# Optimization experiments

Hardware: AMD Instinct MI355X
Metric: run time of the kernel (lower is better)

The kernel has to match this reference:

```python
import jax, jax.numpy as jnp
import numpy as np

N = 100000      # nodes
E = 1600000     # edges (avg degree 16)
IN = 128        # in_channels
HID = 32        # hidden_channels per head
HEADS = 4
OUT = 64        # out_channels
NEG_SLOPE = 0.2 # PyG GATConv default leaky_relu slope


def setup_inputs() -> dict:
    key = jax.random.key(0)
    ks = jax.random.split(key, 12)
    def glorot(k, shape):
        fan = shape[0] + shape[-1]
        s = jnp.sqrt(6.0 / fan)
        return jax.random.uniform(k, shape, jnp.float32, -s, s)
    return {
        "x": jax.random.normal(ks[0], (N, IN), jnp.float32),
        "edge_index": jax.random.randint(ks[1], (2, E), 0, N, dtype=jnp.int64),
        # GATConv layer 1: in=IN, out=HID per head, heads=HEADS, concat=True
        "W1": glorot(ks[2], (IN, HEADS * HID)),
        "a_src1": glorot(ks[3], (HEADS, HID)),
        "a_dst1": glorot(ks[4], (HEADS, HID)),
        "b1": jnp.zeros((HEADS * HID,), jnp.float32),
        # GATConv layer 2: in=HEADS*HID, out=OUT, heads=1, concat=False
        "W2": glorot(ks[5], (HEADS * HID, OUT)),
        "a_src2": glorot(ks[6], (1, OUT)),
        "a_dst2": glorot(ks[7], (1, OUT)),
        "b2": jnp.zeros((OUT,), jnp.float32),
    }


def _gat_layer(x, src, dst, W, a_src, a_dst, bias, num_nodes, concat):
    """PyG-style GATConv (add_self_loops already applied to src/dst).
    x: [N, F_in]; src/dst: [E']; W: [F_in, H*C]; a_*: [H, C]."""
    H, C = a_src.shape
    h = (x @ W).reshape(-1, H, C)                       # [N, H, C]
    # per-node attention scores (avoid gathering full features for logits)
    e_src = (h * a_src[None]).sum(-1)                   # [N, H]
    e_dst = (h * a_dst[None]).sum(-1)                   # [N, H]
    logits = jax.nn.leaky_relu(e_src[src] + e_dst[dst], NEG_SLOPE)  # [E', H]
    # segment softmax over incoming edges of each destination node
    mx = jax.ops.segment_max(logits, dst, num_segments=num_nodes)   # [N, H]
    ex = jnp.exp(logits - mx[dst])                      # [E', H]
    den = jax.ops.segment_sum(ex, dst, num_segments=num_nodes)      # [N, H]
    alpha = ex / (den[dst] + 1e-16)                     # [E', H]
    # weighted message aggregation
    msg = h[src] * alpha[..., None]                     # [E', H, C]
    out = jax.ops.segment_sum(msg, dst, num_segments=num_nodes)     # [N, H, C]
    if concat:
        out = out.reshape(num_nodes, H * C)
    else:
        out = out.mean(axis=1)
    return out + bias


def reference(x, edge_index, W1, a_src1, a_dst1, b1, W2, a_src2, a_dst2, b2):
    n = x.shape[0]
    loops = jnp.arange(n, dtype=edge_index.dtype)
    src = jnp.concatenate([edge_index[0], loops])       # add self-loops (PyG default)
    dst = jnp.concatenate([edge_index[1], loops])
    # dropout layers are identity in eval mode
    h = _gat_layer(x, src, dst, W1, a_src1, a_dst1, b1, n, concat=True)
    h = jax.nn.elu(h)
    out = _gat_layer(h, src, dst, W2, a_src2, a_dst2, b2, n, concat=False)
    return out
```

## Files before the change

### kernel.cpp

```cpp
#include <hip/hip_runtime.h>
#include <cmath>

#define IN_F 128
#define HID 32
#define HEADS 4
#define OUT_F 64
#define NEG_SLOPE 0.2f
#define MAXSEG 128
#define BSHIFT 7
#define NBMAX 1024
#define CHUNK 8192
#define LDSTRIDE 136

typedef short bfrag8 __attribute__((ext_vector_type(8)));
typedef float facc4 __attribute__((ext_vector_type(4)));

__device__ __forceinline__ int ldidx(const int* ei, int pos, int is64) {
  return is64 ? ei[2 * pos] : ei[pos];
}
__device__ __forceinline__ unsigned short f2b(float f) {
  unsigned u = __float_as_uint(f);
  u += 0x7fffu + ((u >> 16) & 1u);
  return (unsigned short)(u >> 16);
}
__device__ __forceinline__ float b2f_lo(unsigned u) { return __uint_as_float(u << 16); }
__device__ __forceinline__ float b2f_hi(unsigned u) { return __uint_as_float(u & 0xffff0000u); }
__device__ __forceinline__ void wave_lds_fence() {
  asm volatile("s_waitcnt lgkmcnt(0)" ::: "memory");
}

__global__ __launch_bounds__(256) void detect_kernel(const int* __restrict__ ei, int E, int* __restrict__ flag) {
  __shared__ int red[256];
  int acc = 0;
  int limit = E < 4096 ? E : 4096;
  for (int j = threadIdx.x; j < limit; j += 256) acc |= ei[2 * j + 1];
  red[threadIdx.x] = acc;
  __syncthreads();
  for (int s = 128; s > 0; s >>= 1) {
    if ((int)threadIdx.x < s) red[threadIdx.x] |= red[threadIdx.x + s];
    __syncthreads();
  }
  if (threadIdx.x == 0) *flag = (red[0] == 0) ? 1 : 0;
}

__global__ __launch_bounds__(256) void bcount_kernel(const int* __restrict__ ei, int E, int Etot,
                                                     const int* __restrict__ flag, int NB,
                                                     int* __restrict__ bcnt) {
  __shared__ int hcnt[NBMAX];
  int tid = threadIdx.x;
  int base = blockIdx.x * CHUNK;
  int cnt = Etot - base; if (cnt > CHUNK) cnt = CHUNK;
  int is64 = *flag;
  for (int i = tid; i < NB; i += 256) hcnt[i] = 0;
  __syncthreads();
  for (int i = tid; i < cnt; i += 256) {
    int e = base + i;
    int d = (e < E) ? ldidx(ei, E + e, is64) : (e - E);
    atomicAdd(&hcnt[d >> BSHIFT], 1);
  }
  __syncthreads();
  for (int i = tid; i < NB; i += 256) {
    int c = hcnt[i];
    if (c) atomicAdd(&bcnt[i], c);
  }
}

__global__ __launch_bounds__(1024) void bscan_kernel(const int* __restrict__ bcnt,
                                                     int* __restrict__ bptr, int* __restrict__ bcur, int NB) {
  __shared__ int wsum[16];
  int tid = threadIdx.x, lane = tid & 63, w = tid >> 6;
  int v = (tid < NB) ? bcnt[tid] : 0;
  int incl = v;
  #pragma unroll
  for (int off = 1; off < 64; off <<= 1) { int t = __shfl_up(incl, off); if (lane >= off) incl += t; }
  if (lane == 63) wsum[w] = incl;
  __syncthreads();
  if (w == 0) {
    int s = (lane < 16) ? wsum[lane] : 0;
    #pragma unroll
    for (int off = 1; off < 16; off <<= 1) { int t = __shfl_up(s, off); if (lane >= off) s += t; }
    if (lane < 16) wsum[lane] = s;
  }
  __syncthreads();
  if (w > 0) incl += wsum[w - 1];
  int excl = incl - v;
  if (tid < NB) { bptr[tid] = excl; bcur[tid] = excl; }
  if (tid == 1023) bptr[NB] = incl;
}

__global__ __launch_bounds__(256) void bscatter_kernel(const int* __restrict__ ei, int E, int Etot,
                                                       const int* __restrict__ flag, int NB,
                                                       int* __restrict__ bcur, uint2* __restrict__ ebuf) {
  __shared__ int hcnt[NBMAX];
  __shared__ int hcur[NBMAX];
  int tid = threadIdx.x;
  int base = blockIdx.x * CHUNK;
  int cnt = Etot - base; if (cnt > CHUNK) cnt = CHUNK;
  int is64 = *flag;
  for (int i = tid; i < NB; i += 256) hcnt[i] = 0;
  __syncthreads();
  for (int i = tid; i < cnt; i += 256) {
    int e = base + i;
    int d = (e < E) ? ldidx(ei, E + e, is64) : (e - E);
    atomicAdd(&hcnt[d >> BSHIFT], 1);
  }
  __syncthreads();
  for (int i = tid; i < NB; i += 256) {
    int c = hcnt[i];
    hcur[i] = c ? atomicAdd(&bcur[i], c) : 0;
  }
  __syncthreads();
  for (int i = tid; i < cnt; i += 256) {
    int e = base + i;
    int s, d;
    if (e < E) { s = ldidx(ei, e, is64); d = ldidx(ei, E + e, is64); }
    else       { s = e - E; d = s; }
    int pos = atomicAdd(&hcur[d >> BSHIFT], 1);
    ebuf[pos] = make_uint2((unsigned)s, (unsigned)d);
  }
}

__global__ __launch_bounds__(256) void bcsr_kernel(const int* __restrict__ bptr, const uint2* __restrict__ ebuf,
                                                   int* __restrict__ rowptr, int* __restrict__ csr,
                                                   int N, int NB) {
  __shared__ int cnt[128];
  __shared__ int cur[128];
  __shared__ int w0sum;
  int tid = threadIdx.x;
  int b = blockIdx.x;
  int lo = bptr[b], hi = bptr[b + 1];
  int node0 = b << BSHIFT;
  int nn = N - node0; if (nn > 128) nn = 128;
  if (tid < 128) cnt[tid] = 0;
  __syncthreads();
  for (int i = lo + tid; i < hi; i += 256) {
    atomicAdd(&cnt[ebuf[i].y & 127], 1);
  }
  __syncthreads();
  int v = 0, incl = 0;
  if (tid < 128) {
    v = cnt[tid];
    incl = v;
    int lane = tid & 63;
    #pragma unroll
    for (int off = 1; off < 64; off <<= 1) { int t = __shfl_up(incl, off); if (lane >= off) incl += t; }
    if (tid == 63) w0sum = incl;
  }
  __syncthreads();
  if (tid < 128) {
    if (tid >= 64) incl += w0sum;
    int excl = incl - v;
    cur[tid] = excl;
    if (tid < nn) rowptr[node0 + tid] = lo + excl;
  }
  if (b == NB - 1 && tid == 0) rowptr[N] = hi;
  __syncthreads();
  for (int i = lo + tid; i < hi; i += 256) {
    uint2 pr = ebuf[i];
    int p = atomicAdd(&cur[pr.y & 127], 1);
    csr[lo + p] = (int)pr.x;
  }
}

__global__ __launch_bounds__(256) void gemm1_kernel(
    const float* __restrict__ x, const float* __restrict__ W,
    const float* __restrict__ asr, const float* __restrict__ ads,
    unsigned short* __restrict__ h1b, float* __restrict__ es, float* __restrict__ ed,
    int N) {
  __shared__ short Wt[128 * LDSTRIDE];
  __shared__ short As[64 * LDSTRIDE];
  int tid = threadIdx.x;
  int row0 = blockIdx.x * 64;
  int lane = tid & 63, wv = tid >> 6;
  int m2 = lane & 15, quad = lane >> 4;

  for (int i = tid; i < 128 * 128; i += 256) {
    int k = i >> 7, c = i & 127;
    Wt[c * LDSTRIDE + k] = (short)f2b(W[i]);
  }
  for (int idx = tid; idx < 64 * 16; idx += 256) {
    int r = idx >> 4, ch = idx & 15;
    int n = row0 + r;
    bfrag8 sv;
    if (n < N) {
      float4 v0 = *(const float4*)&x[(size_t)n * 128 + ch * 8];
      float4 v1 = *(const float4*)&x[(size_t)n * 128 + ch * 8 + 4];
      sv[0] = (short)f2b(v0.x); sv[1] = (short)f2b(v0.y);
      sv[2] = (short)f2b(v0.z); sv[3] = (short)f2b(v0.w);
      sv[4] = (short)f2b(v1.x); sv[5] = (short)f2b(v1.y);
      sv[6] = (short)f2b(v1.z); sv[7] = (short)f2b(v1.w);
    } else {
      sv = (bfrag8)0;
    }
    *(bfrag8*)&As[r * LDSTRIDE + ch * 8] = sv;
  }
  __syncthreads();

  facc4 acc[8] = {};
  const short* Abase = &As[(wv * 16 + m2) * LDSTRIDE];
  #pragma unroll
  for (int ks = 0; ks < 4; ++ks) {
    int k = ks * 32 + quad * 8;
    bfrag8 af = *(const bfrag8*)&Abase[k];
    #pragma unroll
    for (int t = 0; t < 8; ++t) {
      bfrag8 bf = *(const bfrag8*)&Wt[(t * 16 + m2) * LDSTRIDE + k];
      acc[t] = __builtin_amdgcn_mfma_f32_16x16x32_bf16(af, bf, acc[t], 0, 0, 0);
    }
  }

  float av[8], bv[8];
  #pragma unroll
  for (int t = 0; t < 8; ++t) {
    int ai = (t >> 1) * 32 + (t & 1) * 16 + m2;
    av[t] = asr[ai]; bv[t] = ads[ai];
  }
  #pragma unroll
  for (int r = 0; r < 4; ++r) {
    int n = row0 + wv * 16 + quad * 4 + r;
    bool valid = (n < N);
    if (valid) {
      #pragma unroll
      for (int t = 0; t < 8; ++t)
        h1b[(size_t)n * 128 + t * 16 + m2] = f2b(acc[t][r]);
    }
    #pragma unroll
    for (int h = 0; h < 4; ++h) {
      float ps = acc[2 * h][r] * av[2 * h] + acc[2 * h + 1][r] * av[2 * h + 1];
      float pd = acc[2 * h][r] * bv[2 * h] + acc[2 * h + 1][r] * bv[2 * h + 1];
      ps += __shfl_xor(ps, 1); ps += __shfl_xor(ps, 2); ps += __shfl_xor(ps, 4); ps += __shfl_xor(ps, 8);
      pd += __shfl_xor(pd, 1); pd += __shfl_xor(pd, 2); pd += __shfl_xor(pd, 4); pd += __shfl_xor(pd, 8);
      if (valid && m2 == 0) {
        es[(size_t)n * 4 + h] = ps;
        ed[(size_t)n * 4 + h] = pd;
      }
    }
  }
}

__global__ __launch_bounds__(256) void gemm2_kernel(
    const unsigned short* __restrict__ xb, const float* __restrict__ W,
    const float* __restrict__ asr, const float* __restrict__ ads,
    unsigned short* __restrict__ h2b, float* __restrict__ es, float* __restrict__ ed,
    int N) {
  __shared__ short Wt[64 * LDSTRIDE];
  __shared__ short As[64 * LDSTRIDE];
  int tid = threadIdx.x;
  int row0 = blockIdx.x * 64;
  int lane = tid & 63, wv = tid >> 6;
  int m2 = lane & 15, quad = lane >> 4;

  for (int i = tid; i < 128 * 64; i += 256) {
    int k = i >> 6, c = i & 63;
    Wt[c * LDSTRIDE + k] = (short)f2b(W[i]);
  }
  for (int idx = tid; idx < 64 * 16; idx += 256) {
    int r = idx >> 4, ch = idx & 15;
    int n = row0 + r;
    uint4 u = (n < N) ? *(const uint4*)&xb[(size_t)n * 128 + ch * 8]
                      : make_uint4(0, 0, 0, 0);
    *(uint4*)&As[r * LDSTRIDE + ch * 8] = u;
  }
  __syncthreads();

  facc4 acc[4] = {};
  const short* Abase = &As[(wv * 16 + m2) * LDSTRIDE];
  #pragma unroll
  for (int ks = 0; ks < 4; ++ks) {
    int k = ks * 32 + quad * 8;
    bfrag8 af = *(const bfrag8*)&Abase[k];
    #pragma unroll
    for (int t = 0; t < 4; ++t) {
      bfrag8 bf = *(const bfrag8*)&Wt[(t * 16 + m2) * LDSTRIDE + k];
      acc[t] = __builtin_amdgcn_mfma_f32_16x16x32_bf16(af, bf, acc[t], 0, 0, 0);
    }
  }

  float av[4], bv[4];
  #pragma unroll
  for (int t = 0; t < 4; ++t) {
    av[t] = asr[t * 16 + m2]; bv[t] = ads[t * 16 + m2];
  }
  #pragma unroll
  for (int r = 0; r < 4; ++r) {
    int n = row0 + wv * 16 + quad * 4 + r;
    bool valid = (n < N);
    if (valid) {
      #pragma unroll
      for (int t = 0; t < 4; ++t)
        h2b[(size_t)n * 64 + t * 16 + m2] = f2b(acc[t][r]);
    }
    float ps = acc[0][r] * av[0] + acc[1][r] * av[1] + acc[2][r] * av[2] + acc[3][r] * av[3];
    float pd = acc[0][r] * bv[0] + acc[1][r] * bv[1] + acc[2][r] * bv[2] + acc[3][r] * bv[3];
    ps += __shfl_xor(ps, 1); ps += __shfl_xor(ps, 2); ps += __shfl_xor(ps, 4); ps += __shfl_xor(ps, 8);
    pd += __shfl_xor(pd, 1); pd += __shfl_xor(pd, 2); pd += __shfl_xor(pd, 4); pd += __shfl_xor(pd, 8);
    if (valid && m2 == 0) { es[n] = ps; ed[n] = pd; }
  }
}

__global__ __launch_bounds__(256) void agg1_kernel(
    const int* __restrict__ rowptr, const int* __restrict__ csr,
    const float* __restrict__ es, const float* __restrict__ ed,
    const unsigned short* __restrict__ h1b, const float* __restrict__ b1,
    unsigned short* __restrict__ hmidb, int N) {
  __shared__ float lds_p[4][MAXSEG][4];
  __shared__ int   lds_s[4][MAXSEG];
  int wv = threadIdx.x >> 6, lane = threadIdx.x & 63;
  int n = blockIdx.x * 4 + wv;
  if (n >= N) return;
  int start = rowptr[n], end = rowptr[n + 1];
  int len = end - start;
  float4 edv = ((const float4*)ed)[n];
  int f = lane * 2;
  int hh = lane >> 4;
  float ax = 0.f, ay = 0.f;
  const unsigned* h32 = (const unsigned*)h1b;

  if (len <= MAXSEG) {
    float m0 = -1e30f, m1 = -1e30f, m2 = -1e30f, m3 = -1e30f;
    for (int j = lane; j < len; j += 64) {
      int s = csr[start + j];
      lds_s[wv][j] = s;
      float4 ev = ((const float4*)es)[s];
      float l0 = ev.x + edv.x; l0 = l0 > 0.f ? l0 : NEG_SLOPE * l0;
      float l1 = ev.y + edv.y; l1 = l1 > 0.f ? l1 : NEG_SLOPE * l1;
      float l2 = ev.z + edv.z; l2 = l2 > 0.f ? l2 : NEG_SLOPE * l2;
      float l3 = ev.w + edv.w; l3 = l3 > 0.f ? l3 : NEG_SLOPE * l3;
      *(float4*)&lds_p[wv][j][0] = make_float4(l0, l1, l2, l3);
      m0 = fmaxf(m0, l0); m1 = fmaxf(m1, l1); m2 = fmaxf(m2, l2); m3 = fmaxf(m3, l3);
    }
    #pragma unroll
    for (int off = 32; off; off >>= 1) {
      m0 = fmaxf(m0, __shfl_xor(m0, off)); m1 = fmaxf(m1, __shfl_xor(m1, off));
      m2 = fmaxf(m2, __shfl_xor(m2, off)); m3 = fmaxf(m3, __shfl_xor(m3, off));
    }
    float s0 = 0.f, s1 = 0.f, s2 = 0.f, s3 = 0.f;
    for (int j = lane; j < len; j += 64) {
      float4 l = *(float4*)&lds_p[wv][j][0];
      float p0 = __expf(l.x - m0), p1 = __expf(l.y - m1);
      float p2 = __expf(l.z - m2), p3 = __expf(l.w - m3);
      *(float4*)&lds_p[wv][j][0] = make_float4(p0, p1, p2, p3);
      s0 += p0; s1 += p1; s2 += p2; s3 += p3;
    }
    #pragma unroll
    for (int off = 32; off; off >>= 1) {
      s0 += __shfl_xor(s0, off); s1 += __shfl_xor(s1, off);
      s2 += __shfl_xor(s2, off); s3 += __shfl_xor(s3, off);
    }
    float i0 = 1.f / (s0 + 1e-16f), i1 = 1.f / (s1 + 1e-16f);
    float i2 = 1.f / (s2 + 1e-16f), i3 = 1.f / (s3 + 1e-16f);
    float ih = (hh & 2) ? ((hh & 1) ? i3 : i2) : ((hh & 1) ? i1 : i0);
    wave_lds_fence();
    float ax1 = 0.f, ay1 = 0.f;
    int j = 0;
    for (; j + 4 <= len; j += 4) {
      int sA = lds_s[wv][j],     sB = lds_s[wv][j + 1];
      int sC = lds_s[wv][j + 2], sD = lds_s[wv][j + 3];
      float aA = lds_p[wv][j][hh] * ih,     aB = lds_p[wv][j + 1][hh] * ih;
      float aC = lds_p[wv][j + 2][hh] * ih, aD = lds_p[wv][j + 3][hh] * ih;
      unsigned uA = h32[(size_t)sA * 64 + lane];
      unsigned uB = h32[(size_t)sB * 64 + lane];
      unsigned uC = h32[(size_t)sC * 64 + lane];
      unsigned uD = h32[(size_t)sD * 64 + lane];
      ax  = fmaf(b2f_lo(uA), aA, ax);  ay  = fmaf(b2f_hi(uA), aA, ay);
      ax1 = fmaf(b2f_lo(uB), aB, ax1); ay1 = fmaf(b2f_hi(uB), aB, ay1);
      ax  = fmaf(b2f_lo(uC), aC, ax);  ay  = fmaf(b2f_hi(uC), aC, ay);
      ax1 = fmaf(b2f_lo(uD), aD, ax1); ay1 = fmaf(b2f_hi(uD), aD, ay1);
    }
    for (; j < len; ++j) {
      int sA = lds_s[wv][j];
      float aA = lds_p[wv][j][hh] * ih;
      unsigned uA = h32[(size_t)sA * 64 + lane];
      ax = fmaf(b2f_lo(uA), aA, ax);
      ay = fmaf(b2f_hi(uA), aA, ay);
    }
    ax += ax1; ay += ay1;
  } else {
    float m0 = -1e30f, m1 = -1e30f, m2 = -1e30f, m3 = -1e30f;
    for (int j = start + lane; j < end; j += 64) {
      int s = csr[j];
      float4 ev = ((const float4*)es)[s];
      float l0 = ev.x + edv.x; l0 = l0 > 0.f ? l0 : NEG_SLOPE * l0;
      float l1 = ev.y + edv.y; l1 = l1 > 0.f ? l1 : NEG_SLOPE * l1;
      float l2 = ev.z + edv.z; l2 = l2 > 0.f ? l2 : NEG_SLOPE * l2;
      float l3 = ev.w + edv.w; l3 = l3 > 0.f ? l3 : NEG_SLOPE * l3;
      m0 = fmaxf(m0, l0); m1 = fmaxf(m1, l1); m2 = fmaxf(m2, l2); m3 = fmaxf(m3, l3);
    }
    #pragma unroll
    for (int off = 32; off; off >>= 1) {
      m0 = fmaxf(m0, __shfl_xor(m0, off)); m1 = fmaxf(m1, __shfl_xor(m1, off));
      m2 = fmaxf(m2, __shfl_xor(m2, off)); m3 = fmaxf(m3, __shfl_xor(m3, off));
    }
    float s0 = 0.f, s1 = 0.f, s2 = 0.f, s3 = 0.f;
    for (int j = start + lane; j < end; j += 64) {
      int s = csr[j];
      float4 ev = ((const float4*)es)[s];
      float l0 = ev.x + edv.x; l0 = l0 > 0.f ? l0 : NEG_SLOPE * l0;
      float l1 = ev.y + edv.y; l1 = l1 > 0.f ? l1 : NEG_SLOPE * l1;
      float l2 = ev.z + edv.z; l2 = l2 > 0.f ? l2 : NEG_SLOPE * l2;
      float l3 = ev.w + edv.w; l3 = l3 > 0.f ? l3 : NEG_SLOPE * l3;
      s0 += __expf(l0 - m0); s1 += __expf(l1 - m1); s2 += __expf(l2 - m2); s3 += __expf(l3 - m3);
    }
    #pragma unroll
    for (int off = 32; off; off >>= 1) {
      s0 += __shfl_xor(s0, off); s1 += __shfl_xor(s1, off);
      s2 += __shfl_xor(s2, off); s3 += __shfl_xor(s3, off);
    }
    float i0 = 1.f / (s0 + 1e-16f), i1 = 1.f / (s1 + 1e-16f);
    float i2 = 1.f / (s2 + 1e-16f), i3 = 1.f / (s3 + 1e-16f);
    float edh = (hh & 2) ? ((hh & 1) ? edv.w : edv.z) : ((hh & 1) ? edv.y : edv.x);
    float mh = (hh & 2) ? ((hh & 1) ? m3 : m2) : ((hh & 1) ? m1 : m0);
    float ih = (hh & 2) ? ((hh & 1) ? i3 : i2) : ((hh & 1) ? i1 : i0);
    for (int j = start; j < end; ++j) {
      int s = csr[j];
      float l = es[(size_t)s * 4 + hh] + edh; l = l > 0.f ? l : NEG_SLOPE * l;
      float a = __expf(l - mh) * ih;
      unsigned u = h32[(size_t)s * 64 + lane];
      ax = fmaf(b2f_lo(u), a, ax);
      ay = fmaf(b2f_hi(u), a, ay);
    }
  }
  float o0 = ax + b1[f], o1 = ay + b1[f + 1];
  o0 = o0 > 0.f ? o0 : expm1f(o0);
  o1 = o1 > 0.f ? o1 : expm1f(o1);
  unsigned packed = (unsigned)f2b(o0) | ((unsigned)f2b(o1) << 16);
  ((unsigned*)hmidb)[(size_t)n * 64 + lane] = packed;
}

__global__ __launch_bounds__(256) void agg2_kernel(
    const int* __restrict__ rowptr, const int* __restrict__ csr,
    const float* __restrict__ es, const float* __restrict__ ed,
    const unsigned short* __restrict__ h2b, const float* __restrict__ b2,
    float* __restrict__ out, int N) {
  __shared__ float lds_p[4][MAXSEG];
  __shared__ int   lds_s[4][MAXSEG];
  int wv = threadIdx.x >> 6, lane = threadIdx.x & 63;
  int n = blockIdx.x * 4 + wv;
  if (n >= N) return;
  int start = rowptr[n], end = rowptr[n + 1];
  int len = end - start;
  float edv = ed[n];
  float acc = 0.f;

  if (len <= MAXSEG) {
    float m = -1e30f;
    for (int j = lane; j < len; j += 64) {
      int s = csr[start + j];
      lds_s[wv][j] = s;
      float l = es[s] + edv; l = l > 0.f ? l : NEG_SLOPE * l;
      lds_p[wv][j] = l;
      m = fmaxf(m, l);
    }
    #pragma unroll
    for (int off = 32; off; off >>= 1) m = fmaxf(m, __shfl_xor(m, off));
    float sm = 0.f;
    for (int j = lane; j < len; j += 64) {
      float p = __expf(lds_p[wv][j] - m);
      lds_p[wv][j] = p;
      sm += p;
    }
    #pragma unroll
    for (int off = 32; off; off >>= 1) sm += __shfl_xor(sm, off);
    float inv = 1.f / (sm + 1e-16f);
    wave_lds_fence();
    float acc1 = 0.f;
    int j = 0;
    for (; j + 4 <= len; j += 4) {
      int sA = lds_s[wv][j],     sB = lds_s[wv][j + 1];
      int sC = lds_s[wv][j + 2], sD = lds_s[wv][j + 3];
      float aA = lds_p[wv][j] * inv,     aB = lds_p[wv][j + 1] * inv;
      float aC = lds_p[wv][j + 2] * inv, aD = lds_p[wv][j + 3] * inv;
      float vA = __uint_as_float(((unsigned)h2b[(size_t)sA * 64 + lane]) << 16);
      float vB = __uint_as_float(((unsigned)h2b[(size_t)sB * 64 + lane]) << 16);
      float vC = __uint_as_float(((unsigned)h2b[(size_t)sC * 64 + lane]) << 16);
      float vD = __uint_as_float(((unsigned)h2b[(size_t)sD * 64 + lane]) << 16);
      acc  = fmaf(vA, aA, acc);  acc1 = fmaf(vB, aB, acc1);
      acc  = fmaf(vC, aC, acc);  acc1 = fmaf(vD, aD, acc1);
    }
    for (; j < len; ++j) {
      int sA = lds_s[wv][j];
      float aA = lds_p[wv][j] * inv;
      float vA = __uint_as_float(((unsigned)h2b[(size_t)sA * 64 + lane]) << 16);
      acc = fmaf(vA, aA, acc);
    }
    acc += acc1;
  } else {
    float m = -1e30f;
    for (int j = start + lane; j < end; j += 64) {
      float l = es[csr[j]] + edv; l = l > 0.f ? l : NEG_SLOPE * l;
      m = fmaxf(m, l);
    }
    #pragma unroll
    for (int off = 32; off; off >>= 1) m = fmaxf(m, __shfl_xor(m, off));
    float sm = 0.f;
    for (int j = start + lane; j < end; j += 64) {
      float l = es[csr[j]] + edv; l = l > 0.f ? l : NEG_SLOPE * l;
      sm += __expf(l - m);
    }
    #pragma unroll
    for (int off = 32; off; off >>= 1) sm += __shfl_xor(sm, off);
    float inv = 1.f / (sm + 1e-16f);
    for (int j = start; j < end; ++j) {
      int s = csr[j];
      float l = es[s] + edv; l = l > 0.f ? l : NEG_SLOPE * l;
      float a = __expf(l - m) * inv;
      float v = __uint_as_float(((unsigned)h2b[(size_t)s * 64 + lane]) << 16);
      acc = fmaf(v, a, acc);
    }
  }
  out[(size_t)n * 64 + lane] = acc + b2[lane];
}

extern "C" void kernel_launch(void* const* d_in, const int* in_sizes, int n_in,
                              void* d_out, int out_size, void* d_ws, size_t ws_size,
                              hipStream_t stream) {
  const float* x   = (const float*)d_in[0];
  const int*   ei  = (const int*)d_in[1];
  const float* W1  = (const float*)d_in[2];
  const float* as1 = (const float*)d_in[3];
  const float* ad1 = (const float*)d_in[4];
  const float* b1  = (const float*)d_in[5];
  const float* W2  = (const float*)d_in[6];
  const float* as2 = (const float*)d_in[7];
  const float* ad2 = (const float*)d_in[8];
  const float* b2  = (const float*)d_in[9];
  float* out = (float*)d_out;

  int N = in_sizes[0] / IN_F;
  int E = in_sizes[1] / 2;
  int Etot = E + N;
  int NB = (N + 127) >> BSHIFT;

  char* p = (char*)d_ws;
  auto carve = [&](size_t bytes) -> char* {
    char* r = p;
    p += (bytes + 255) & ~(size_t)255;
    return r;
  };
  int* flag     = (int*)carve(4);
  int* bcnt     = (int*)carve((size_t)NBMAX * 4);
  int* bptr     = (int*)carve((size_t)(NBMAX + 1) * 4);
  int* bcur     = (int*)carve((size_t)NBMAX * 4);
  uint2* ebuf   = (uint2*)carve((size_t)Etot * 8);
  int* rowptr   = (int*)carve((size_t)(N + 1) * 4);
  int* csr      = (int*)carve((size_t)Etot * 4);
  float* es1    = (float*)carve((size_t)N * 4 * 4);
  float* ed1    = (float*)carve((size_t)N * 4 * 4);
  float* es2    = (float*)carve((size_t)N * 4);
  float* ed2    = (float*)carve((size_t)N * 4);
  unsigned short* h1b   = (unsigned short*)carve((size_t)N * 128 * 2);
  unsigned short* hmidb = (unsigned short*)carve((size_t)N * 128 * 2);
  unsigned short* h2b   = (unsigned short*)carve((size_t)N * 64 * 2);

  int nchunk = (Etot + CHUNK - 1) / CHUNK;
  hipMemsetAsync(bcnt, 0, (size_t)NB * 4, stream);
  detect_kernel<<<1, 256, 0, stream>>>(ei, E, flag);
  bcount_kernel<<<nchunk, 256, 0, stream>>>(ei, E, Etot, flag, NB, bcnt);
  bscan_kernel<<<1, 1024, 0, stream>>>(bcnt, bptr, bcur, NB);
  bscatter_kernel<<<nchunk, 256, 0, stream>>>(ei, E, Etot, flag, NB, bcur, ebuf);
  bcsr_kernel<<<NB, 256, 0, stream>>>(bptr, ebuf, rowptr, csr, N, NB);
  gemm1_kernel<<<(N + 63) / 64, 256, 0, stream>>>(x, W1, as1, ad1, h1b, es1, ed1, N);
  agg1_kernel<<<(N + 3) / 4, 256, 0, stream>>>(rowptr, csr, es1, ed1, h1b, b1, hmidb, N);
  gemm2_kernel<<<(N + 63) / 64, 256, 0, stream>>>(hmidb, W2, as2, ad2, h2b, es2, ed2, N);
  agg2_kernel<<<(N + 3) / 4, 256, 0, stream>>>(rowptr, csr, es2, ed2, h2b, b2, out, N);
}
```

Measured before the change: 354.9 us.

## Process four nodes per wave in aggregation kernels and pack edge buffer

Both aggregation kernels now give each wave four destination nodes. The softmax runs per 16-lane group, and the gather loop handles two edges at once, with each half-wave reading a wider slice of a feature row. Before, one node per wave wasted most lanes, since the average degree is about 17. The bucket-scatter buffer also packs source and local destination into a single 32-bit word, which halves that traffic. In exchange the code is more complex, and nodes with degree above 64 fall back to a slow serial path that runs after the fast loop.

```diff
diff --git a/kernel.cpp b/kernel.cpp
--- a/kernel.cpp
+++ b/kernel.cpp
@@ -2,11 +2,8 @@
 #include <cmath>
 
 #define IN_F 128
-#define HID 32
-#define HEADS 4
-#define OUT_F 64
 #define NEG_SLOPE 0.2f
-#define MAXSEG 128
+#define SEG 64
 #define BSHIFT 7
 #define NBMAX 1024
 #define CHUNK 8192
@@ -28,6 +25,7 @@
 __device__ __forceinline__ void wave_lds_fence() {
   asm volatile("s_waitcnt lgkmcnt(0)" ::: "memory");
 }
+__device__ __forceinline__ float leaky(float l) { return fmaxf(l, NEG_SLOPE * l); }
 
 __global__ __launch_bounds__(256) void detect_kernel(const int* __restrict__ ei, int E, int* __restrict__ flag) {
   __shared__ int red[256];
@@ -90,7 +88,7 @@
 
 __global__ __launch_bounds__(256) void bscatter_kernel(const int* __restrict__ ei, int E, int Etot,
                                                        const int* __restrict__ flag, int NB,
-                                                       int* __restrict__ bcur, uint2* __restrict__ ebuf) {
+                                                       int* __restrict__ bcur, unsigned* __restrict__ ebuf) {
   __shared__ int hcnt[NBMAX];
   __shared__ int hcur[NBMAX];
   int tid = threadIdx.x;
@@ -116,11 +114,11 @@
     if (e < E) { s = ldidx(ei, e, is64); d = ldidx(ei, E + e, is64); }
     else       { s = e - E; d = s; }
     int pos = atomicAdd(&hcur[d >> BSHIFT], 1);
-    ebuf[pos] = make_uint2((unsigned)s, (unsigned)d);
-  }
-}
-
-__global__ __launch_bounds__(256) void bcsr_kernel(const int* __restrict__ bptr, const uint2* __restrict__ ebuf,
+    ebuf[pos] = ((unsigned)s << 7) | ((unsigned)d & 127u);
+  }
+}
+
+__global__ __launch_bounds__(256) void bcsr_kernel(const int* __restrict__ bptr, const unsigned* __restrict__ ebuf,
                                                    int* __restrict__ rowptr, int* __restrict__ csr,
                                                    int N, int NB) {
   __shared__ int cnt[128];
@@ -134,7 +132,7 @@
   if (tid < 128) cnt[tid] = 0;
   __syncthreads();
   for (int i = lo + tid; i < hi; i += 256) {
-    atomicAdd(&cnt[ebuf[i].y & 127], 1);
+    atomicAdd(&cnt[ebuf[i] & 127u], 1);
   }
   __syncthreads();
   int v = 0, incl = 0;
@@ -156,9 +154,9 @@
   if (b == NB - 1 && tid == 0) rowptr[N] = hi;
   __syncthreads();
   for (int i = lo + tid; i < hi; i += 256) {
-    uint2 pr = ebuf[i];
-    int p = atomicAdd(&cur[pr.y & 127], 1);
-    csr[lo + p] = (int)pr.x;
+    unsigned pr = ebuf[i];
+    int p = atomicAdd(&cur[pr & 127u], 1);
+    csr[lo + p] = (int)(pr >> 7);
   }
 }
 
@@ -301,214 +299,300 @@
 __global__ __launch_bounds__(256) void agg1_kernel(
     const int* __restrict__ rowptr, const int* __restrict__ csr,
     const float* __restrict__ es, const float* __restrict__ ed,
-    const unsigned short* __restrict__ h1b, const float* __restrict__ b1,
+    const unsigned short* __restrict__ h1b, const float* __restrict__ bias1,
     unsigned short* __restrict__ hmidb, int N) {
-  __shared__ float lds_p[4][MAXSEG][4];
-  __shared__ int   lds_s[4][MAXSEG];
-  int wv = threadIdx.x >> 6, lane = threadIdx.x & 63;
-  int n = blockIdx.x * 4 + wv;
-  if (n >= N) return;
-  int start = rowptr[n], end = rowptr[n + 1];
-  int len = end - start;
-  float4 edv = ((const float4*)ed)[n];
-  int f = lane * 2;
-  int hh = lane >> 4;
-  float ax = 0.f, ay = 0.f;
-  const unsigned* h32 = (const unsigned*)h1b;
-
-  if (len <= MAXSEG) {
+  __shared__ float lds_a[4][4][4][SEG + 1];
+  __shared__ int   lds_s[4][4][SEG];
+  int tid = threadIdx.x;
+  int wv = tid >> 6, lane = tid & 63;
+  int sub = lane >> 4, sj = lane & 15;
+  int nbase = blockIdx.x * 16 + wv * 4;
+  int n = nbase + sub;
+  bool nvalid = (n < N);
+  int start = 0, len = 0;
+  if (nvalid) { start = rowptr[n]; len = rowptr[n + 1] - start; }
+  int lenc = (len <= SEG) ? len : 0;
+
+  float4 edv = nvalid ? ((const float4*)ed)[n] : make_float4(0.f, 0.f, 0.f, 0.f);
+  float l[4][4];
+  float mx = -1e30f;
+  #pragma unroll
+  for (int it = 0; it < 4; ++it) {
+    int j = sj + it * 16;
+    if (j < lenc) {
+      int s = csr[start + j];
+      lds_s[wv][sub][j] = s;
+      float4 ev = ((const float4*)es)[s];
+      float l0 = leaky(ev.x + edv.x);
+      float l1 = leaky(ev.y + edv.y);
+      float l2 = leaky(ev.z + edv.z);
+      float l3 = leaky(ev.w + edv.w);
+      l[it][0] = l0; l[it][1] = l1; l[it][2] = l2; l[it][3] = l3;
+      mx = fmaxf(mx, fmaxf(fmaxf(l0, l1), fmaxf(l2, l3)));
+    } else {
+      l[it][0] = -1e30f; l[it][1] = -1e30f; l[it][2] = -1e30f; l[it][3] = -1e30f;
+    }
+  }
+  #pragma unroll
+  for (int off = 1; off < 16; off <<= 1) mx = fmaxf(mx, __shfl_xor(mx, off));
+
+  float s0 = 0.f, s1 = 0.f, s2 = 0.f, s3 = 0.f;
+  #pragma unroll
+  for (int it = 0; it < 4; ++it) {
+    float p0 = __expf(l[it][0] - mx);
+    float p1 = __expf(l[it][1] - mx);
+    float p2 = __expf(l[it][2] - mx);
+    float p3 = __expf(l[it][3] - mx);
+    l[it][0] = p0; l[it][1] = p1; l[it][2] = p2; l[it][3] = p3;
+    s0 += p0; s1 += p1; s2 += p2; s3 += p3;
+  }
+  #pragma unroll
+  for (int off = 1; off < 16; off <<= 1) {
+    s0 += __shfl_xor(s0, off); s1 += __shfl_xor(s1, off);
+    s2 += __shfl_xor(s2, off); s3 += __shfl_xor(s3, off);
+  }
+  float i0 = __builtin_amdgcn_rcpf(s0 + 1e-16f);
+  float i1 = __builtin_amdgcn_rcpf(s1 + 1e-16f);
+  float i2 = __builtin_amdgcn_rcpf(s2 + 1e-16f);
+  float i3 = __builtin_amdgcn_rcpf(s3 + 1e-16f);
+  #pragma unroll
+  for (int it = 0; it < 4; ++it) {
+    int j = sj + it * 16;
+    if (j < lenc) {
+      lds_a[wv][sub][0][j] = l[it][0] * i0;
+      lds_a[wv][sub][1][j] = l[it][1] * i1;
+      lds_a[wv][sub][2][j] = l[it][2] * i2;
+      lds_a[wv][sub][3][j] = l[it][3] * i3;
+    }
+  }
+  if (sj == 0 && (lenc & 1)) {
+    lds_s[wv][sub][lenc] = 0;
+    lds_a[wv][sub][0][lenc] = 0.f; lds_a[wv][sub][1][lenc] = 0.f;
+    lds_a[wv][sub][2][lenc] = 0.f; lds_a[wv][sub][3][lenc] = 0.f;
+  }
+  wave_lds_fence();
+
+  int fl = lane & 31, eidx = lane >> 5, hd = fl >> 3;
+  const uint2* hrow = (const uint2*)h1b;
+  #pragma unroll 1
+  for (int i = 0; i < 4; ++i) {
+    int lenC = __shfl(lenc, i << 4);
+    if (lenC == 0) continue;
+    int nI = nbase + i;
+    const float* aP = &lds_a[wv][i][hd][0];
+    const int*   sP = &lds_s[wv][i][0];
+    int lenp = (lenC + 1) & ~1;
+    float c0 = 0.f, c1 = 0.f, c2 = 0.f, c3 = 0.f;
+    float d0 = 0.f, d1 = 0.f, d2 = 0.f, d3 = 0.f;
+    int g = 0;
+    for (; g + 4 <= lenp; g += 4) {
+      int sA = sP[g + eidx],     sB = sP[g + 2 + eidx];
+      float wA = aP[g + eidx],   wB = aP[g + 2 + eidx];
+      uint2 uA = hrow[(size_t)sA * 32 + fl];
+      uint2 uB = hrow[(size_t)sB * 32 + fl];
+      c0 = fmaf(b2f_lo(uA.x), wA, c0); c1 = fmaf(b2f_hi(uA.x), wA, c1);
+      c2 = fmaf(b2f_lo(uA.y), wA, c2); c3 = fmaf(b2f_hi(uA.y), wA, c3);
+      d0 = fmaf(b2f_lo(uB.x), wB, d0); d1 = fmaf(b2f_hi(uB.x), wB, d1);
+      d2 = fmaf(b2f_lo(uB.y), wB, d2); d3 = fmaf(b2f_hi(uB.y), wB, d3);
+    }
+    if (g < lenp) {
+      int sA = sP[g + eidx];
+      float wA = aP[g + eidx];
+      uint2 uA = hrow[(size_t)sA * 32 + fl];
+      c0 = fmaf(b2f_lo(uA.x), wA, c0); c1 = fmaf(b2f_hi(uA.x), wA, c1);
+      c2 = fmaf(b2f_lo(uA.y), wA, c2); c3 = fmaf(b2f_hi(uA.y), wA, c3);
+    }
+    c0 += d0; c1 += d1; c2 += d2; c3 += d3;
+    c0 += __shfl_xor(c0, 32); c1 += __shfl_xor(c1, 32);
+    c2 += __shfl_xor(c2, 32); c3 += __shfl_xor(c3, 32);
+    if (eidx == 0) {
+      float4 bb = *(const float4*)&bias1[fl * 4];
+      float o0 = c0 + bb.x, o1 = c1 + bb.y, o2 = c2 + bb.z, o3 = c3 + bb.w;
+      o0 = o0 > 0.f ? o0 : expm1f(o0);
+      o1 = o1 > 0.f ? o1 : expm1f(o1);
+      o2 = o2 > 0.f ? o2 : expm1f(o2);
+      o3 = o3 > 0.f ? o3 : expm1f(o3);
+      uint2 pk;
+      pk.x = (unsigned)f2b(o0) | ((unsigned)f2b(o1) << 16);
+      pk.y = (unsigned)f2b(o2) | ((unsigned)f2b(o3) << 16);
+      ((uint2*)hmidb)[(size_t)nI * 32 + fl] = pk;
+    }
+  }
+
+  #pragma unroll 1
+  for (int i = 0; i < 4; ++i) {
+    int lenF = __shfl(len, i << 4);
+    if (lenF <= SEG) continue;
+    int stF = __shfl(start, i << 4);
+    int nI = nbase + i;
+    float4 ed4 = ((const float4*)ed)[nI];
+    int f = lane * 2, hh = lane >> 4;
+    const unsigned* h32 = (const unsigned*)h1b;
     float m0 = -1e30f, m1 = -1e30f, m2 = -1e30f, m3 = -1e30f;
-    for (int j = lane; j < len; j += 64) {
-      int s = csr[start + j];
-      lds_s[wv][j] = s;
+    for (int j = stF + lane; j < stF + lenF; j += 64) {
+      int s = csr[j];
       float4 ev = ((const float4*)es)[s];
-      float l0 = ev.x + edv.x; l0 = l0 > 0.f ? l0 : NEG_SLOPE * l0;
-      float l1 = ev.y + edv.y; l1 = l1 > 0.f ? l1 : NEG_SLOPE * l1;
-      float l2 = ev.z + edv.z; l2 = l2 > 0.f ? l2 : NEG_SLOPE * l2;
-      float l3 = ev.w + edv.w; l3 = l3 > 0.f ? l3 : NEG_SLOPE * l3;
-      *(float4*)&lds_p[wv][j][0] = make_float4(l0, l1, l2, l3);
-      m0 = fmaxf(m0, l0); m1 = fmaxf(m1, l1); m2 = fmaxf(m2, l2); m3 = fmaxf(m3, l3);
+      m0 = fmaxf(m0, leaky(ev.x + ed4.x)); m1 = fmaxf(m1, leaky(ev.y + ed4.y));
+      m2 = fmaxf(m2, leaky(ev.z + ed4.z)); m3 = fmaxf(m3, leaky(ev.w + ed4.w));
     }
     #pragma unroll
     for (int off = 32; off; off >>= 1) {
       m0 = fmaxf(m0, __shfl_xor(m0, off)); m1 = fmaxf(m1, __shfl_xor(m1, off));
       m2 = fmaxf(m2, __shfl_xor(m2, off)); m3 = fmaxf(m3, __shfl_xor(m3, off));
     }
-    float s0 = 0.f, s1 = 0.f, s2 = 0.f, s3 = 0.f;
-    for (int j = lane; j < len; j += 64) {
-      float4 l = *(float4*)&lds_p[wv][j][0];
-      float p0 = __expf(l.x - m0), p1 = __expf(l.y - m1);
-      float p2 = __expf(l.z - m2), p3 = __expf(l.w - m3);
-      *(float4*)&lds_p[wv][j][0] = make_float4(p0, p1, p2, p3);
-      s0 += p0; s1 += p1; s2 += p2; s3 += p3;
-    }
-    #pragma unroll
-    for (int off = 32; off; off >>= 1) {
-      s0 += __shfl_xor(s0, off); s1 += __shfl_xor(s1, off);
-      s2 += __shfl_xor(s2, off); s3 += __shfl_xor(s3, off);
-    }
-    float i0 = 1.f / (s0 + 1e-16f), i1 = 1.f / (s1 + 1e-16f);
-    float i2 = 1.f / (s2 + 1e-16f), i3 = 1.f / (s3 + 1e-16f);
-    float ih = (hh & 2) ? ((hh & 1) ? i3 : i2) : ((hh & 1) ? i1 : i0);
-    wave_lds_fence();
-    float ax1 = 0.f, ay1 = 0.f;
-    int j = 0;
-    for (; j + 4 <= len; j += 4) {
-      int sA = lds_s[wv][j],     sB = lds_s[wv][j + 1];
-      int sC = lds_s[wv][j + 2], sD = lds_s[wv][j + 3];
-      float aA = lds_p[wv][j][hh] * ih,     aB = lds_p[wv][j + 1][hh] * ih;
-      float aC = lds_p[wv][j + 2][hh] * ih, aD = lds_p[wv][j + 3][hh] * ih;
-      unsigned uA = h32[(size_t)sA * 64 + lane];
-      unsigned uB = h32[(size_t)sB * 64 + lane];
-      unsigned uC = h32[(size_t)sC * 64 + lane];
-      unsigned uD = h32[(size_t)sD * 64 + lane];
-      ax  = fmaf(b2f_lo(uA), aA, ax);  ay  = fmaf(b2f_hi(uA), aA, ay);
-      ax1 = fmaf(b2f_lo(uB), aB, ax1); ay1 = fmaf(b2f_hi(uB), aB, ay1);
-      ax  = fmaf(b2f_lo(uC), aC, ax);  ay  = fmaf(b2f_hi(uC), aC, ay);
-      ax1 = fmaf(b2f_lo(uD), aD, ax1); ay1 = fmaf(b2f_hi(uD), aD, ay1);
-    }
-    for (; j < len; ++j) {
-      int sA = lds_s[wv][j];
-      float aA = lds_p[wv][j][hh] * ih;
-      unsigned uA = h32[(size_t)sA * 64 + lane];
-      ax = fmaf(b2f_lo(uA), aA, ax);
-      ay = fmaf(b2f_hi(uA), aA, ay);
-    }
-    ax += ax1; ay += ay1;
-  } else {
-    float m0 = -1e30f, m1 = -1e30f, m2 = -1e30f, m3 = -1e30f;
-    for (int j = start + lane; j < end; j += 64) {
+    float t0 = 0.f, t1 = 0.f, t2 = 0.f, t3 = 0.f;
+    for (int j = stF + lane; j < stF + lenF; j += 64) {
       int s = csr[j];
       float4 ev = ((const float4*)es)[s];
-      float l0 = ev.x + edv.x; l0 = l0 > 0.f ? l0 : NEG_SLOPE * l0;
-      float l1 = ev.y + edv.y; l1 = l1 > 0.f ? l1 : NEG_SLOPE * l1;
-      float l2 = ev.z + edv.z; l2 = l2 > 0.f ? l2 : NEG_SLOPE * l2;
-      float l3 = ev.w + edv.w; l3 = l3 > 0.f ? l3 : NEG_SLOPE * l3;
-      m0 = fmaxf(m0, l0); m1 = fmaxf(m1, l1); m2 = fmaxf(m2, l2); m3 = fmaxf(m3, l3);
+      t0 += __expf(leaky(ev.x + ed4.x) - m0); t1 += __expf(leaky(ev.y + ed4.y) - m1);
+      t2 += __expf(leaky(ev.z + ed4.z) - m2); t3 += __expf(leaky(ev.w + ed4.w) - m3);
     }
     #pragma unroll
     for (int off = 32; off; off >>= 1) {
-      m0 = fmaxf(m0, __shfl_xor(m0, off)); m1 = fmaxf(m1, __shfl_xor(m1, off));
-      m2 = fmaxf(m2, __shfl_xor(m2, off)); m3 = fmaxf(m3, __shfl_xor(m3, off));
-    }
-    float s0 = 0.f, s1 = 0.f, s2 = 0.f, s3 = 0.f;
-    for (int j = start + lane; j < end; j += 64) {
+      t0 += __shfl_xor(t0, off); t1 += __shfl_xor(t1, off);
+      t2 += __shfl_xor(t2, off); t3 += __shfl_xor(t3, off);
+    }
+    float j0 = 1.f / (t0 + 1e-16f), j1 = 1.f / (t1 + 1e-16f);
+    float j2 = 1.f / (t2 + 1e-16f), j3 = 1.f / (t3 + 1e-16f);
+    float edh = (hh & 2) ? ((hh & 1) ? ed4.w : ed4.z) : ((hh & 1) ? ed4.y : ed4.x);
+    float mh  = (hh & 2) ? ((hh & 1) ? m3 : m2) : ((hh & 1) ? m1 : m0);
+    float ih  = (hh & 2) ? ((hh & 1) ? j3 : j2) : ((hh & 1) ? j1 : j0);
+    float ax = 0.f, ay = 0.f;
+    for (int j = stF; j < stF + lenF; ++j) {
       int s = csr[j];
-      float4 ev = ((const float4*)es)[s];
-      float l0 = ev.x + edv.x; l0 = l0 > 0.f ? l0 : NEG_SLOPE * l0;
-      float l1 = ev.y + edv.y; l1 = l1 > 0.f ? l1 : NEG_SLOPE * l1;
-      float l2 = ev.z + edv.z; l2 = l2 > 0.f ? l2 : NEG_SLOPE * l2;
-      float l3 = ev.w + edv.w; l3 = l3 > 0.f ? l3 : NEG_SLOPE * l3;
-      s0 += __expf(l0 - m0); s1 += __expf(l1 - m1); s2 += __expf(l2 - m2); s3 += __expf(l3 - m3);
-    }
-    #pragma unroll
-    for (int off = 32; off; off >>= 1) {
-      s0 += __shfl_xor(s0, off); s1 += __shfl_xor(s1, off);
-      s2 += __shfl_xor(s2, off); s3 += __shfl_xor(s3, off);
-    }
-    float i0 = 1.f / (s0 + 1e-16f), i1 = 1.f / (s1 + 1e-16f);
-    float i2 = 1.f / (s2 + 1e-16f), i3 = 1.f / (s3 + 1e-16f);
-    float edh = (hh & 2) ? ((hh & 1) ? edv.w : edv.z) : ((hh & 1) ? edv.y : edv.x);
-    float mh = (hh & 2) ? ((hh & 1) ? m3 : m2) : ((hh & 1) ? m1 : m0);
-    float ih = (hh & 2) ? ((hh & 1) ? i3 : i2) : ((hh & 1) ? i1 : i0);
-    for (int j = start; j < end; ++j) {
-      int s = csr[j];
-      float l = es[(size_t)s * 4 + hh] + edh; l = l > 0.f ? l : NEG_SLOPE * l;
-      float a = __expf(l - mh) * ih;
+      float lv = leaky(es[(size_t)s * 4 + hh] + edh);
+      float a = __expf(lv - mh) * ih;
       unsigned u = h32[(size_t)s * 64 + lane];
       ax = fmaf(b2f_lo(u), a, ax);
       ay = fmaf(b2f_hi(u), a, ay);
     }
-  }
-  float o0 = ax + b1[f], o1 = ay + b1[f + 1];
-  o0 = o0 > 0.f ? o0 : expm1f(o0);
-  o1 = o1 > 0.f ? o1 : expm1f(o1);
-  unsigned packed = (unsigned)f2b(o0) | ((unsigned)f2b(o1) << 16);
-  ((unsigned*)hmidb)[(size_t)n * 64 + lane] = packed;
+    float o0 = ax + bias1[f], o1 = ay + bias1[f + 1];
+    o0 = o0 > 0.f ? o0 : expm1f(o0);
+    o1 = o1 > 0.f ? o1 : expm1f(o1);
+    unsigned packed = (unsigned)f2b(o0) | ((unsigned)f2b(o1) << 16);
+    ((unsigned*)hmidb)[(size_t)nI * 64 + lane] = packed;
+  }
 }
 
 __global__ __launch_bounds__(256) void agg2_kernel(
     const int* __restrict__ rowptr, const int* __restrict__ csr,
     const float* __restrict__ es, const float* __restrict__ ed,
-    const unsigned short* __restrict__ h2b, const float* __restrict__ b2,
+    const unsigned short* __restrict__ h2b, const float* __restrict__ bias2,
     float* __restrict__ out, int N) {
-  __shared__ float lds_p[4][MAXSEG];
-  __shared__ int   lds_s[4][MAXSEG];
-  int wv = threadIdx.x >> 6, lane = threadIdx.x & 63;
-  int n = blockIdx.x * 4 + wv;
-  if (n >= N) return;
-  int start = rowptr[n], end = rowptr[n + 1];
-  int len = end - start;
-  float edv = ed[n];
-  float acc = 0.f;
-
-  if (len <= MAXSEG) {
+  __shared__ float lds_a[4][4][SEG + 2];
+  __shared__ int   lds_s[4][4][SEG];
+  int tid = threadIdx.x;
+  int wv = tid >> 6, lane = tid & 63;
+  int sub = lane >> 4, sj = lane & 15;
+  int nbase = blockIdx.x * 16 + wv * 4;
+  int n = nbase + sub;
+  bool nvalid = (n < N);
+  int start = 0, len = 0;
+  if (nvalid) { start = rowptr[n]; len = rowptr[n + 1] - start; }
+  int lenc = (len <= SEG) ? len : 0;
+
+  float edv = nvalid ? ed[n] : 0.f;
+  float l[4];
+  float mx = -1e30f;
+  #pragma unroll
+  for (int it = 0; it < 4; ++it) {
+    int j = sj + it * 16;
+    if (j < lenc) {
+      int s = csr[start + j];
+      lds_s[wv][sub][j] = s;
+      float lv = leaky(es[s] + edv);
+      l[it] = lv;
+      mx = fmaxf(mx, lv);
+    } else {
+      l[it] = -1e30f;
+    }
+  }
+  #pragma unroll
+  for (int off = 1; off < 16; off <<= 1) mx = fmaxf(mx, __shfl_xor(mx, off));
+  float sm = 0.f;
+  #pragma unroll
+  for (int it = 0; it < 4; ++it) {
+    float p = __expf(l[it] - mx);
+    l[it] = p;
+    sm += p;
+  }
+  #pragma unroll
+  for (int off = 1; off < 16; off <<= 1) sm += __shfl_xor(sm, off);
+  float inv = __builtin_amdgcn_rcpf(sm + 1e-16f);
+  #pragma unroll
+  for (int it = 0; it < 4; ++it) {
+    int j = sj + it * 16;
+    if (j < lenc) lds_a[wv][sub][j] = l[it] * inv;
+  }
+  if (sj == 0 && (lenc & 1)) {
+    lds_s[wv][sub][lenc] = 0;
+    lds_a[wv][sub][lenc] = 0.f;
+  }
+  wave_lds_fence();
+
+  int fl = lane & 31, eidx = lane >> 5;
+  const unsigned* hrow = (const unsigned*)h2b;
+  #pragma unroll 1
+  for (int i = 0; i < 4; ++i) {
+    int lenC = __shfl(lenc, i << 4);
+    if (lenC == 0) continue;
+    int nI = nbase + i;
+    const float* aP = &lds_a[wv][i][0];
+    const int*   sP = &lds_s[wv][i][0];
+    int lenp = (lenC + 1) & ~1;
+    float c0 = 0.f, c1 = 0.f, d0 = 0.f, d1 = 0.f;
+    int g = 0;
+    for (; g + 4 <= lenp; g += 4) {
+      int sA = sP[g + eidx],   sB = sP[g + 2 + eidx];
+      float wA = aP[g + eidx], wB = aP[g + 2 + eidx];
+      unsigned uA = hrow[(size_t)sA * 32 + fl];
+      unsigned uB = hrow[(size_t)sB * 32 + fl];
+      c0 = fmaf(b2f_lo(uA), wA, c0); c1 = fmaf(b2f_hi(uA), wA, c1);
+      d0 = fmaf(b2f_lo(uB), wB, d0); d1 = fmaf(b2f_hi(uB), wB, d1);
+    }
+    if (g < lenp) {
+      int sA = sP[g + eidx];
+      float wA = aP[g + eidx];
+      unsigned uA = hrow[(size_t)sA * 32 + fl];
+      c0 = fmaf(b2f_lo(uA), wA, c0); c1 = fmaf(b2f_hi(uA), wA, c1);
+    }
+    c0 += d0; c1 += d1;
+    c0 += __shfl_xor(c0, 32); c1 += __shfl_xor(c1, 32);
+    if (eidx == 0) {
+      float2 bb = *(const float2*)&bias2[fl * 2];
+      ((float2*)out)[(size_t)nI * 32 + fl] = make_float2(c0 + bb.x, c1 + bb.y);
+    }
+  }
+
+  #pragma unroll 1
+  for (int i = 0; i < 4; ++i) {
+    int lenF = __shfl(len, i << 4);
+    if (lenF <= SEG) continue;
+    int stF = __shfl(start, i << 4);
+    int nI = nbase + i;
+    float edF = ed[nI];
     float m = -1e30f;
-    for (int j = lane; j < len; j += 64) {
-      int s = csr[start + j];
-      lds_s[wv][j] = s;
-      float l = es[s] + edv; l = l > 0.f ? l : NEG_SLOPE * l;
-      lds_p[wv][j] = l;
-      m = fmaxf(m, l);
+    for (int j = stF + lane; j < stF + lenF; j += 64) {
+      m = fmaxf(m, leaky(es[csr[j]] + edF));
     }
     #pragma unroll
     for (int off = 32; off; off >>= 1) m = fmaxf(m, __shfl_xor(m, off));
-    float sm = 0.f;
-    for (int j = lane; j < len; j += 64) {
-      float p = __expf(lds_p[wv][j] - m);
-      lds_p[wv][j] = p;
-      sm += p;
-    }
-    #pragma unroll
-    for (int off = 32; off; off >>= 1) sm += __shfl_xor(sm, off);
-    float inv = 1.f / (sm + 1e-16f);
-    wave_lds_fence();
-    float acc1 = 0.f;
-    int j = 0;
-    for (; j + 4 <= len; j += 4) {
-      int sA = lds_s[wv][j],     sB = lds_s[wv][j + 1];
-      int sC = lds_s[wv][j + 2], sD = lds_s[wv][j + 3];
-      float aA = lds_p[wv][j] * inv,     aB = lds_p[wv][j + 1] * inv;
-      float aC = lds_p[wv][j + 2] * inv, aD = lds_p[wv][j + 3] * inv;
-      float vA = __uint_as_float(((unsigned)h2b[(size_t)sA * 64 + lane]) << 16);
-      float vB = __uint_as_float(((unsigned)h2b[(size_t)sB * 64 + lane]) << 16);
-      float vC = __uint_as_float(((unsigned)h2b[(size_t)sC * 64 + lane]) << 16);
-      float vD = __uint_as_float(((unsigned)h2b[(size_t)sD * 64 + lane]) << 16);
-      acc  = fmaf(vA, aA, acc);  acc1 = fmaf(vB, aB, acc1);
-      acc  = fmaf(vC, aC, acc);  acc1 = fmaf(vD, aD, acc1);
-    }
-    for (; j < len; ++j) {
-      int sA = lds_s[wv][j];
-      float aA = lds_p[wv][j] * inv;
-      float vA = __uint_as_float(((unsigned)h2b[(size_t)sA * 64 + lane]) << 16);
-      acc = fmaf(vA, aA, acc);
-    }
-    acc += acc1;
-  } else {
-    float m = -1e30f;
-    for (int j = start + lane; j < end; j += 64) {
-      float l = es[csr[j]] + edv; l = l > 0.f ? l : NEG_SLOPE * l;
-      m = fmaxf(m, l);
-    }
-    #pragma unroll
-    for (int off = 32; off; off >>= 1) m = fmaxf(m, __shfl_xor(m, off));
-    float sm = 0.f;
-    for (int j = start + lane; j < end; j += 64) {
-      float l = es[csr[j]] + edv; l = l > 0.f ? l : NEG_SLOPE * l;
-      sm += __expf(l - m);
-    }
-    #pragma unroll
-    for (int off = 32; off; off >>= 1) sm += __shfl_xor(sm, off);
-    float inv = 1.f / (sm + 1e-16f);
-    for (int j = start; j < end; ++j) {
+    float t = 0.f;
+    for (int j = stF + lane; j < stF + lenF; j += 64) {
+      t += __expf(leaky(es[csr[j]] + edF) - m);
+    }
+    #pragma unroll
+    for (int off = 32; off; off >>= 1) t += __shfl_xor(t, off);
+    float iv = 1.f / (t + 1e-16f);
+    float acc = 0.f;
+    for (int j = stF; j < stF + lenF; ++j) {
       int s = csr[j];
-      float l = es[s] + edv; l = l > 0.f ? l : NEG_SLOPE * l;
-      float a = __expf(l - m) * inv;
+      float a = __expf(leaky(es[s] + edF) - m) * iv;
       float v = __uint_as_float(((unsigned)h2b[(size_t)s * 64 + lane]) << 16);
       acc = fmaf(v, a, acc);
     }
-  }
-  out[(size_t)n * 64 + lane] = acc + b2[lane];
+    out[(size_t)nI * 64 + lane] = acc + bias2[lane];
+  }
 }
 
 extern "C" void kernel_launch(void* const* d_in, const int* in_sizes, int n_in,
@@ -541,7 +625,7 @@
   int* bcnt     = (int*)carve((size_t)NBMAX * 4);
   int* bptr     = (int*)carve((size_t)(NBMAX + 1) * 4);
   int* bcur     = (int*)carve((size_t)NBMAX * 4);
-  uint2* ebuf   = (uint2*)carve((size_t)Etot * 8);
+  unsigned* ebuf = (unsigned*)carve((size_t)Etot * 4);
   int* rowptr   = (int*)carve((size_t)(N + 1) * 4);
   int* csr      = (int*)carve((size_t)Etot * 4);
   float* es1    = (float*)carve((size_t)N * 4 * 4);
@@ -560,7 +644,7 @@
   bscatter_kernel<<<nchunk, 256, 0, stream>>>(ei, E, Etot, flag, NB, bcur, ebuf);
   bcsr_kernel<<<NB, 256, 0, stream>>>(bptr, ebuf, rowptr, csr, N, NB);
   gemm1_kernel<<<(N + 63) / 64, 256, 0, stream>>>(x, W1, as1, ad1, h1b, es1, ed1, N);
-  agg1_kernel<<<(N + 3) / 4, 256, 0, stream>>>(rowptr, csr, es1, ed1, h1b, b1, hmidb, N);
+  agg1_kernel<<<(N + 15) / 16, 256, 0, stream>>>(rowptr, csr, es1, ed1, h1b, b1, hmidb, N);
   gemm2_kernel<<<(N + 63) / 64, 256, 0, stream>>>(hmidb, W2, as2, ad2, h2b, es2, ed2, N);
-  agg2_kernel<<<(N + 3) / 4, 256, 0, stream>>>(rowptr, csr, es2, ed2, h2b, b2, out, N);
-}
+  agg2_kernel<<<(N + 15) / 16, 256, 0, stream>>>(rowptr, csr, es2, ed2, h2b, b2, out, N);
+}
```

After: 342.1 us. 3.6% less time.
